# Kernel optimization log

Measured on AMD Instinct MI355X. Metric: run time of the kernel, lower is better.

Reference implementation:

```python
import jax, jax.numpy as jnp
import numpy as np

# Sizes derived from init_kwargs via calc_mlp_features:
# total_param=2117777, router_ratio=0.002 -> router_param=4235.554, expert_param=264192
# expert_hidden = 256, router_hidden = 352
N = 131072      # number of coordinate points
CIN = 3         # expert_insize == router_insize (xyz coords)
E = 8           # num_experts
K = 2           # top_k
H = 256         # expert_hidden (also SIREN data_channel)
RH = 352        # router_hidden
NHID = 3        # expert_layers - 2 hidden SIREN layers
W0C = 30.0      # sine frequency w0


def setup_inputs() -> dict:
    key = jax.random.key(0)
    ks = jax.random.split(key, 16)
    u = lambda k, shape, a: jax.random.uniform(k, shape, jnp.float32, -a, a)
    x = jax.random.uniform(ks[0], (N, CIN), jnp.float32, -1.0, 1.0)
    context = jax.random.uniform(ks[1], (N, CIN), jnp.float32, -1.0, 1.0)
    # Router: kaiming-normal weights, torch-default uniform biases
    Wr1 = jax.random.normal(ks[2], (CIN, RH), jnp.float32) * np.float32(np.sqrt(2.0 / CIN))
    br1 = u(ks[3], (RH,), 1.0 / np.sqrt(CIN))
    Wr2 = jax.random.normal(ks[4], (RH, E), jnp.float32) * np.float32(np.sqrt(2.0 / RH))
    br2 = u(ks[5], (E,), 1.0 / np.sqrt(RH))
    # SIREN experts (stacked over E): first layer U(-1/in, 1/in), rest U(+-sqrt(6/in)/30)
    sb = np.sqrt(6.0 / H) / 30.0
    W0 = u(ks[6], (E, CIN, H), 1.0 / CIN)
    b0 = u(ks[7], (E, H), 1.0 / np.sqrt(CIN))
    Wh = u(ks[8], (E, NHID, H, H), sb)
    bh = u(ks[9], (E, NHID, H), 1.0 / np.sqrt(H))
    Wo = u(ks[10], (E, H, H), sb)
    bo = u(ks[11], (E, H), 1.0 / np.sqrt(H))
    # Decoder: Linear(H,H)+ReLU+Linear(H,1)
    Wd1 = jax.random.normal(ks[12], (H, H), jnp.float32) * np.float32(np.sqrt(2.0 / H))
    bd1 = u(ks[13], (H,), 1.0 / np.sqrt(H))
    Wd2 = jax.random.normal(ks[14], (H, 1), jnp.float32) * np.float32(np.sqrt(2.0 / H))
    bd2 = u(ks[15], (1,), 1.0 / np.sqrt(H))
    return dict(x=x, context=context, Wr1=Wr1, br1=br1, Wr2=Wr2, br2=br2,
                W0=W0, b0=b0, Wh=Wh, bh=bh, Wo=Wo, bo=bo,
                Wd1=Wd1, bd1=bd1, Wd2=Wd2, bd2=bd2)


def reference(x, context, Wr1, br1, Wr2, br2, W0, b0, Wh, bh, Wo, bo, Wd1, bd1, Wd2, bd2):
    n = x.shape[0]
    # --- NoisyTopkRouter (eval path: no noise) ---
    logits = jnp.maximum(context @ Wr1 + br1, 0.0) @ Wr2 + br2          # [N, E]
    topv, topi = jax.lax.top_k(logits, K)                                # [N, K]
    # softmax over -inf-filled sparse logits == softmax over the top-k values
    w = jax.nn.softmax(topv, axis=-1)                                    # [N, K]
    gating = jnp.zeros_like(logits).at[jnp.arange(n)[:, None], topi].set(w)  # [N, E], zero off top-k
    # --- Per-expert SIREN, weighted combine ---
    # Masked dispatch + scatter-add in the original equals dense weighted sum
    # because gating is exactly zero for non-selected experts.
    def expert_step(acc, p):
        W0e, b0e, Whe, bhe, Woe, boe, ge = p
        h = jnp.sin(W0C * (x @ W0e + b0e))                # [N, H]
        for i in range(NHID):
            h = jnp.sin(W0C * (h @ Whe[i] + bhe[i]))
        out = h @ Woe + boe                               # [N, H], no output activation
        return acc + out * ge[:, None], None
    acc0 = jnp.zeros((n, H), dtype=x.dtype)
    final, _ = jax.lax.scan(expert_step, acc0, (W0, b0, Wh, bh, Wo, bo, gating.T))
    # --- Decoder ---
    return jnp.maximum(final @ Wd1 + bd1, 0.0) @ Wd2 + bd2               # [N, 1]
```

## Files before the change

kernel.cpp:

```cpp
#include <hip/hip_runtime.h>
#include <stdint.h>

#define N_PTS 131072
#define RH    352
#define BM    256
#define BME   64
#define TPB   512
#define SREV  4.774648292756860f

typedef short  bf16x8 __attribute__((ext_vector_type(8)));
typedef float  f32x16 __attribute__((ext_vector_type(16)));

__device__ __forceinline__ unsigned short f2bf(float f) {
  uint32_t u = __builtin_bit_cast(uint32_t, f);
  u = (u + 0x7FFFu + ((u >> 16) & 1u)) >> 16;
  return (unsigned short)u;
}
__device__ __forceinline__ float bf2f(unsigned short s) {
  return __builtin_bit_cast(float, ((uint32_t)s) << 16);
}
__device__ __forceinline__ float vsin1(float x) {
  float xf = x - floorf(x);
  float r;
  asm("v_sin_f32 %0, %1" : "=v"(r) : "v"(xf));
  return r;
}
__device__ __forceinline__ void ldsload16(const void* g, void* ldsWaveBase) {
  typedef __attribute__((address_space(3))) uint8_t lds_b;
  typedef __attribute__((address_space(1))) uint8_t glob_b;
  __builtin_amdgcn_global_load_lds((const glob_b*)g, (lds_b*)ldsWaveBase, 16, 0, 0);
}
__device__ __forceinline__ f32x16 mfma_bf16(bf16x8 a, bf16x8 b, f32x16 c) {
  return __builtin_amdgcn_mfma_f32_32x32x16_bf16(a, b, c, 0, 0, 0);
}

#define AWLOAD(d0, d1, addr64) \
  asm volatile("global_load_dwordx4 %0, %2, off\n\t" \
               "global_load_dwordx4 %1, %2, off offset:1024" \
               : "=&v"(d0), "=&v"(d1) : "v"(addr64))

#define VWAIT(N, r0, r1) \
  asm volatile("s_waitcnt vmcnt(" #N ")" : "+v"(r0), "+v"(r1))

__global__ __launch_bounds__(512) void pack_kernel(
    const float* __restrict__ W0, const float* __restrict__ b0,
    const float* __restrict__ Wh, const float* __restrict__ bh,
    const float* __restrict__ Wo, const float* __restrict__ bo,
    const float* __restrict__ Wd1, const float* __restrict__ bd1,
    short* __restrict__ pW0, short* __restrict__ pWh,
    short* __restrict__ pWo, short* __restrict__ pWd1)
{
  int b = blockIdx.x, tid = threadIdx.x;
  int jb = tid >> 6, l = tid & 63;
  int j  = jb*32 + (l & 31);
  int s0 = (l >> 5) * 8;
  unsigned short o[8];
  short* dp;

  if (b < 544) {
    int m = b / 17, slice = b % 17;
    int e = m >> 2, t = m & 3;
    const float* src; const float* bias; float scale; short* dst;
    if (t < 3) { src = Wh + (size_t)(e*3+t)*65536; bias = bh + (size_t)(e*3+t)*256; scale = SREV; dst = pWh + (size_t)(e*3+t)*69632; }
    else       { src = Wo + (size_t)e*65536;       bias = bo + (size_t)e*256;       scale = 1.0f; dst = pWo + (size_t)e*69632; }
    if (slice < 16) {
      #pragma unroll
      for (int i = 0; i < 8; ++i) {
        int k = slice*16 + s0 + i;
        o[i] = f2bf(scale * src[(size_t)k*256 + j]);
      }
    } else {
      #pragma unroll
      for (int i = 0; i < 8; ++i) o[i] = 0;
      if (s0 == 0) {
        float a = scale * bias[j];
        unsigned short h = f2bf(a);
        o[0] = h; o[1] = f2bf(a - bf2f(h));
      }
    }
    dp = dst + (size_t)slice*4096 + jb*512 + l*8;
  } else if (b < 552) {
    int e = b - 544;
    const float* w0 = W0 + (size_t)e*768;
    const float* bb = b0 + (size_t)e*256;
    #pragma unroll
    for (int i = 0; i < 8; ++i) {
      int s = s0 + i;
      unsigned short v = 0;
      if (s < 3) v = f2bf(SREV * w0[(size_t)s*256 + j]);
      else if (s < 6) { float a = SREV * w0[(size_t)(s-3)*256 + j]; unsigned short h = f2bf(a); v = f2bf(a - bf2f(h)); }
      else if (s < 9) v = f2bf(SREV * w0[(size_t)(s-6)*256 + j]);
      else if (s == 9)  v = f2bf(SREV * bb[j]);
      else if (s == 10) { float a = SREV * bb[j]; unsigned short h = f2bf(a); v = f2bf(a - bf2f(h)); }
      o[i] = v;
    }
    dp = pW0 + (size_t)e*4096 + jb*512 + l*8;
  } else {
    int slice = b - 552;
    if (slice < 16) {
      #pragma unroll
      for (int i = 0; i < 8; ++i) {
        int k = slice*16 + s0 + i;
        o[i] = f2bf(Wd1[(size_t)k*256 + j]);
      }
    } else {
      #pragma unroll
      for (int i = 0; i < 8; ++i) o[i] = 0;
      if (s0 == 0) {
        float a = bd1[j];
        unsigned short h = f2bf(a);
        o[0] = h; o[1] = f2bf(a - bf2f(h));
      }
    }
    dp = pWd1 + (size_t)slice*4096 + jb*512 + l*8;
  }
  uint4 v;
  v.x = (uint32_t)o[0] | ((uint32_t)o[1] << 16);
  v.y = (uint32_t)o[2] | ((uint32_t)o[3] << 16);
  v.z = (uint32_t)o[4] | ((uint32_t)o[5] << 16);
  v.w = (uint32_t)o[6] | ((uint32_t)o[7] << 16);
  *(uint4*)dp = v;
}

__global__ __launch_bounds__(256) void router_kernel(
    const float* __restrict__ ctx, const float* __restrict__ Wr1,
    const float* __restrict__ br1, const float* __restrict__ Wr2,
    const float* __restrict__ br2, uint4* __restrict__ topk,
    uint32_t* __restrict__ counts)
{
  __shared__ double w1d[RH*4];
  __shared__ double w2d[RH*8];
  __shared__ uint32_t lcnt[8];
  int tid = threadIdx.x;
  for (int i = tid; i < RH; i += 256) {
    w1d[i*4+0] = (double)Wr1[i];
    w1d[i*4+1] = (double)Wr1[352 + i];
    w1d[i*4+2] = (double)Wr1[704 + i];
    w1d[i*4+3] = (double)br1[i];
  }
  for (int i = tid; i < RH*8; i += 256) w2d[i] = (double)Wr2[i];
  if (tid < 8) lcnt[tid] = 0;
  __syncthreads();

  int n = blockIdx.x*256 + tid;
  double c0 = (double)ctx[(size_t)n*3+0];
  double c1 = (double)ctx[(size_t)n*3+1];
  double c2 = (double)ctx[(size_t)n*3+2];
  double lg[8];
  #pragma unroll
  for (int e = 0; e < 8; ++e) lg[e] = (double)br2[e];
  for (int j = 0; j < RH; ++j) {
    const double* a = &w1d[j*4];
    double h = c0*a[0] + c1*a[1] + c2*a[2] + a[3];
    h = h > 0.0 ? h : 0.0;
    const double* bq = &w2d[j*8];
    lg[0] += h*bq[0]; lg[1] += h*bq[1]; lg[2] += h*bq[2]; lg[3] += h*bq[3];
    lg[4] += h*bq[4]; lg[5] += h*bq[5]; lg[6] += h*bq[6]; lg[7] += h*bq[7];
  }
  double v0 = -1e300, v1 = -1e300; int i0 = 0, i1 = 0;
  #pragma unroll
  for (int e = 0; e < 8; ++e) {
    double lv = lg[e];
    if (lv > v0)      { v1 = v0; i1 = i0; v0 = lv; i0 = e; }
    else if (lv > v1) { v1 = lv; i1 = e; }
  }
  float ex = __expf((float)(v1 - v0));
  float s = 1.0f / (1.0f + ex);
  uint4 t;
  t.x = (uint32_t)i0 | ((uint32_t)i1 << 8);
  t.y = __builtin_bit_cast(uint32_t, s);
  t.z = __builtin_bit_cast(uint32_t, ex * s);
  t.w = 0;
  topk[n] = t;
  atomicAdd(&lcnt[i0], 1u); atomicAdd(&lcnt[i1], 1u);
  __syncthreads();
  if (tid < 8) atomicAdd(&counts[tid], lcnt[tid]);
}

__global__ void scan_kernel(const uint32_t* __restrict__ counts,
                            uint32_t* __restrict__ offsets,
                            uint32_t* __restrict__ cursors)
{
  if (threadIdx.x == 0) {
    uint32_t o = 0;
    for (int e = 0; e < 8; ++e) { offsets[e] = o; cursors[e] = o; o += counts[e]; }
    offsets[8] = o;
  }
}

__global__ __launch_bounds__(256) void scatter_kernel(
    const uint4* __restrict__ topk, uint32_t* __restrict__ cursors,
    uint32_t* __restrict__ plist, float* __restrict__ pw)
{
  __shared__ uint32_t lc[8], lb[8];
  int tid = threadIdx.x;
  if (tid < 8) lc[tid] = 0;
  __syncthreads();
  int n = blockIdx.x*256 + tid;
  uint4 t = topk[n];
  uint32_t e0 = t.x & 255u, e1 = (t.x >> 8) & 255u;
  uint32_t p0 = atomicAdd(&lc[e0], 1u);
  uint32_t p1 = atomicAdd(&lc[e1], 1u);
  __syncthreads();
  if (tid < 8) lb[tid] = atomicAdd(&cursors[tid], lc[tid]);
  __syncthreads();
  uint32_t d0 = lb[e0] + p0, d1 = lb[e1] + p1;
  plist[d0] = ((uint32_t)n << 1);      pw[d0] = __builtin_bit_cast(float, t.y);
  plist[d1] = ((uint32_t)n << 1) | 1u; pw[d1] = __builtin_bit_cast(float, t.z);
}

#define LDS_EXPERT 67584

__global__ __launch_bounds__(256, 2) void expert_kernel(
    const float* __restrict__ x, const uint32_t* __restrict__ counts,
    const uint32_t* __restrict__ offsets, const uint32_t* __restrict__ plist,
    const float* __restrict__ pw, const short* __restrict__ pW0,
    const short* __restrict__ pWh, const short* __restrict__ pWo,
    short* __restrict__ outbuf)
{
  extern __shared__ __align__(16) uint8_t smem[];
  uint8_t* hB0 = smem;
  uint8_t* hB1 = smem + 32768;
  uint8_t* xB  = smem + 65536;

  int tid = threadIdx.x;
  int lane = tid & 63;
  int jq = tid >> 6;
  int aoff = jq*2048 + lane*16;

  bf16x8 bbias;
  #pragma unroll
  for (int i = 0; i < 8; ++i) bbias[i] = 0;
  if (lane < 32) { bbias[0] = (short)0x3F80; bbias[1] = (short)0x3F80; }

  bf16x8 aw[5][2];
  f32x16 acc[2][2];

  int rr = tid >> 2;
  int rq = tid & 3;

  uint32_t tt = blockIdx.x;
  int e = -1; uint32_t cnt = 0;
  #pragma unroll 1
  for (int ee = 0; ee < 8; ++ee) {
    uint32_t c = counts[ee];
    uint32_t nt = (c + (BME-1)) >> 6;
    if (tt < nt) { e = ee; cnt = c; break; }
    tt -= nt;
  }
  if (e < 0) return;
  uint32_t base = offsets[e] + (tt << 6);
  int nvalid = (int)cnt - (int)(tt << 6); if (nvalid > BME) nvalid = BME;

  uint64_t matp[4];
  matp[0] = (uint64_t)(uintptr_t)(pWh + (size_t)(e*3+0)*69632);
  matp[1] = (uint64_t)(uintptr_t)(pWh + (size_t)(e*3+1)*69632);
  matp[2] = (uint64_t)(uintptr_t)(pWh + (size_t)(e*3+2)*69632);
  matp[3] = (uint64_t)(uintptr_t)(pWo + (size_t)e*69632);

  {
    uint64_t pb = matp[0] + (uint64_t)aoff;
    AWLOAD(aw[0][0], aw[0][1], pb);
    AWLOAD(aw[1][0], aw[1][1], pb + 8192);
    AWLOAD(aw[2][0], aw[2][1], pb + 16384);
    AWLOAD(aw[3][0], aw[3][1], pb + 24576);
  }

  float wgt[2];
  #pragma unroll
  for (int c = 0; c < 2; ++c) {
    int n = c*32 + (lane & 31);
    wgt[c] = (n < nvalid) ? pw[base + n] : 0.0f;
  }
  uint32_t psv = (rr < nvalid) ? plist[base + rr] : 0u;

  if (tid < BME) {
    float x0 = 0.0f, x1 = 0.0f, x2 = 0.0f;
    if (tid < nvalid) {
      uint32_t v = plist[base + tid];
      const float* xp = x + (size_t)(v >> 1)*3;
      x0 = xp[0]; x1 = xp[1]; x2 = xp[2];
    }
    unsigned short h0 = f2bf(x0), h1 = f2bf(x1), h2 = f2bf(x2);
    unsigned short l0 = f2bf(x0 - bf2f(h0)), l1 = f2bf(x1 - bf2f(h1)), l2 = f2bf(x2 - bf2f(h2));
    uint4 r0, r1;
    r0.x = (uint32_t)h0 | ((uint32_t)h1 << 16);
    r0.y = (uint32_t)h2 | ((uint32_t)h0 << 16);
    r0.z = (uint32_t)h1 | ((uint32_t)h2 << 16);
    r0.w = (uint32_t)l0 | ((uint32_t)l1 << 16);
    r1.x = (uint32_t)l2 | (0x3F80u << 16);
    r1.y = 0x3F80u;
    r1.z = 0u; r1.w = 0u;
    uint4* dst = (uint4*)(xB + tid*32);
    dst[0] = r0; dst[1] = r1;
  }

  const uint8_t* pw0e = (const uint8_t*)(pW0 + (size_t)e*4096);
  bf16x8 a0[2];
  a0[0] = *(const bf16x8*)(pw0e + aoff);
  a0[1] = *(const bf16x8*)(pw0e + aoff + 1024);

  __syncthreads();

  #pragma unroll
  for (int a2 = 0; a2 < 2; ++a2)
    #pragma unroll
    for (int c = 0; c < 2; ++c)
      #pragma unroll
      for (int r = 0; r < 16; ++r) acc[a2][c][r] = 0.0f;

  {
    bf16x8 bv[2];
    #pragma unroll
    for (int c = 0; c < 2; ++c) {
      int n = c*32 + (lane & 31);
      bv[c] = *(const bf16x8*)(xB + n*32 + ((lane >> 5)*16));
    }
    #pragma unroll
    for (int a2 = 0; a2 < 2; ++a2)
      #pragma unroll
      for (int c = 0; c < 2; ++c)
        acc[a2][c] = mfma_bf16(a0[a2], bv[c], acc[a2][c]);
  }

#define WRITE_SIN(HB) { _Pragma("unroll") \
    for (int a2 = 0; a2 < 2; ++a2) { \
      int jb = jq*2 + a2; \
      _Pragma("unroll") \
      for (int c = 0; c < 2; ++c) { \
        int n = c*32 + (lane & 31); \
        uint32_t rowb = (uint32_t)n * 512u; \
        uint32_t sw = (uint32_t)((n & 7) << 4); \
        _Pragma("unroll") \
        for (int g = 0; g < 4; ++g) { \
          float s0f = vsin1(acc[a2][c][g*4+0]); \
          float s1f = vsin1(acc[a2][c][g*4+1]); \
          float s2f = vsin1(acc[a2][c][g*4+2]); \
          float s3f = vsin1(acc[a2][c][g*4+3]); \
          uint2 pv; \
          pv.x = (uint32_t)f2bf(s0f) | ((uint32_t)f2bf(s1f) << 16); \
          pv.y = (uint32_t)f2bf(s2f) | ((uint32_t)f2bf(s3f) << 16); \
          int j0 = jb*32 + g*8 + ((lane >> 5) << 2); \
          uint32_t off = (rowb + (uint32_t)(j0*2)) ^ sw; \
          *(uint2*)((HB) + off) = pv; \
        } \
      } \
    } }

  WRITE_SIN(hB0);
  __syncthreads();

#define STEP(L, kb, HB) { \
    enum { u_ = (L)*17 + (kb), ps_ = u_ + 4, us_ = u_ % 5, pss_ = ps_ % 5 }; \
    if (ps_ <= 67) { \
      uint64_t pa_ = matp[ps_/17] + (uint64_t)((ps_%17)*8192) + (uint64_t)aoff; \
      AWLOAD(aw[pss_][0], aw[pss_][1], pa_); \
    } \
    if (u_ <= 63)      { VWAIT(8, aw[us_][0], aw[us_][1]); } \
    else if (u_ == 64) { VWAIT(6, aw[us_][0], aw[us_][1]); } \
    else if (u_ == 65) { VWAIT(4, aw[us_][0], aw[us_][1]); } \
    else if (u_ == 66) { VWAIT(2, aw[us_][0], aw[us_][1]); } \
    else               { VWAIT(0, aw[us_][0], aw[us_][1]); } \
    bf16x8 bv0_, bv1_; \
    if ((kb) < 16) { \
      { int n_ = (lane & 31); \
        uint32_t off_ = ((uint32_t)n_*512u + (uint32_t)((kb)*32) + (uint32_t)((lane >> 5)*16)) \
                        ^ (uint32_t)((n_ & 7) << 4); \
        bv0_ = *(const bf16x8*)((HB) + off_); } \
      { int n_ = 32 + (lane & 31); \
        uint32_t off_ = ((uint32_t)n_*512u + (uint32_t)((kb)*32) + (uint32_t)((lane >> 5)*16)) \
                        ^ (uint32_t)((n_ & 7) << 4); \
        bv1_ = *(const bf16x8*)((HB) + off_); } \
    } else { bv0_ = bbias; bv1_ = bbias; } \
    acc[0][0] = mfma_bf16(aw[us_][0], bv0_, acc[0][0]); \
    acc[1][0] = mfma_bf16(aw[us_][1], bv0_, acc[1][0]); \
    acc[0][1] = mfma_bf16(aw[us_][0], bv1_, acc[0][1]); \
    acc[1][1] = mfma_bf16(aw[us_][1], bv1_, acc[1][1]); \
}
#define LAYER17(L, HB) STEP(L,0,HB) STEP(L,1,HB) STEP(L,2,HB) STEP(L,3,HB) \
    STEP(L,4,HB) STEP(L,5,HB) STEP(L,6,HB) STEP(L,7,HB) STEP(L,8,HB) \
    STEP(L,9,HB) STEP(L,10,HB) STEP(L,11,HB) STEP(L,12,HB) STEP(L,13,HB) \
    STEP(L,14,HB) STEP(L,15,HB) STEP(L,16,HB)

#define ZACC() { _Pragma("unroll") for (int a2 = 0; a2 < 2; ++a2) \
    _Pragma("unroll") for (int c = 0; c < 2; ++c) \
    _Pragma("unroll") for (int r = 0; r < 16; ++r) acc[a2][c][r] = 0.0f; }

  ZACC(); LAYER17(0, hB0) WRITE_SIN(hB1); __syncthreads();
  ZACC(); LAYER17(1, hB1) WRITE_SIN(hB0); __syncthreads();
  ZACC(); LAYER17(2, hB0) WRITE_SIN(hB1); __syncthreads();
  ZACC(); LAYER17(3, hB1)
  #pragma unroll
  for (int a2 = 0; a2 < 2; ++a2) {
    int jb = jq*2 + a2;
    #pragma unroll
    for (int c = 0; c < 2; ++c) {
      int n = c*32 + (lane & 31);
      float w = wgt[c];
      uint32_t rowb = (uint32_t)n * 512u;
      uint32_t sw = (uint32_t)((n & 7) << 4);
      #pragma unroll
      for (int g = 0; g < 4; ++g) {
        float s0f = acc[a2][c][g*4+0] * w;
        float s1f = acc[a2][c][g*4+1] * w;
        float s2f = acc[a2][c][g*4+2] * w;
        float s3f = acc[a2][c][g*4+3] * w;
        uint2 pv;
        pv.x = (uint32_t)f2bf(s0f) | ((uint32_t)f2bf(s1f) << 16);
        pv.y = (uint32_t)f2bf(s2f) | ((uint32_t)f2bf(s3f) << 16);
        int j0 = jb*32 + g*8 + ((lane >> 5) << 2);
        uint32_t off = (rowb + (uint32_t)(j0*2)) ^ sw;
        *(uint2*)(hB0 + off) = pv;
      }
    }
  }
  __syncthreads();
  if (rr < nvalid) {
    uint4* dst = (uint4*)(outbuf + ((size_t)(psv & 1)*N_PTS + (size_t)(psv >> 1))*256
                          + rq*64);
    uint32_t rowb = (uint32_t)rr*512u + (uint32_t)rq*128u;
    uint32_t sw = (uint32_t)((rr & 7) << 4);
    #pragma unroll
    for (int c = 0; c < 8; ++c)
      dst[c] = *(const uint4*)(hB0 + ((rowb + (uint32_t)(c*16)) ^ sw));
  }
}

#define LDS_DEC 150528

__global__ __launch_bounds__(TPB, 2) void decoder_kernel(
    const short* __restrict__ outbuf, const short* __restrict__ pWd1,
    const float* __restrict__ Wd2v, const float* __restrict__ bd2,
    float* __restrict__ outp)
{
  extern __shared__ __align__(16) uint8_t smem[];
  uint8_t* hB = smem;
  uint8_t* wB = smem + 131072;
  float* wd2 = (float*)(smem + 147456);
  float* part = (float*)(smem + 148480);

  int tid = threadIdx.x;
  int lane = tid & 63;
  int wv = tid >> 6;
  int nw = wv & 3;
  int jw = wv >> 2;
  int tbase = blockIdx.x * BM;

  ldsload16((const uint8_t*)pWd1 + (size_t)tid*16, wB + (tid >> 6)*1024);
  if (tid < 256) wd2[tid] = Wd2v[tid];

  const short* o0 = outbuf + (size_t)tbase*256;
  const short* o1 = outbuf + ((size_t)N_PTS + tbase)*256;
  #pragma unroll 1
  for (int it = 0; it < 16; ++it) {
    int c = it*512 + tid;
    uint4 a  = *(const uint4*)(o0 + (size_t)c*8);
    uint4 bq = *(const uint4*)(o1 + (size_t)c*8);
    uint4 ov;
    uint32_t* ap = (uint32_t*)&a;
    uint32_t* bp = (uint32_t*)&bq;
    uint32_t* op = (uint32_t*)&ov;
    #pragma unroll
    for (int w = 0; w < 4; ++w) {
      uint32_t ua = ap[w], ub = bp[w];
      float f0 = bf2f((unsigned short)(ua & 0xFFFFu)) + bf2f((unsigned short)(ub & 0xFFFFu));
      float f1 = bf2f((unsigned short)(ua >> 16))     + bf2f((unsigned short)(ub >> 16));
      op[w] = (uint32_t)f2bf(f0) | ((uint32_t)f2bf(f1) << 16);
    }
    int n = c >> 5;
    uint32_t off = ((uint32_t)n*512u + (uint32_t)(c & 31)*16u) ^ (uint32_t)((n & 7) << 4);
    *(uint4*)(hB + off) = ov;
  }
  __syncthreads();

  f32x16 acc[4][2];
  #pragma unroll
  for (int a2 = 0; a2 < 4; ++a2)
    #pragma unroll
    for (int c = 0; c < 2; ++c)
      #pragma unroll
      for (int r = 0; r < 16; ++r) acc[a2][c][r] = 0.0f;
  bf16x8 bbias;
  #pragma unroll
  for (int i = 0; i < 8; ++i) bbias[i] = 0;
  if (lane < 32) { bbias[0] = (short)0x3F80; bbias[1] = (short)0x3F80; }

  #pragma unroll 1
  for (int kb = 0; kb < 17; ++kb) {
    if (kb < 16)
      ldsload16((const uint8_t*)(pWd1 + (size_t)(kb+1)*4096) + (size_t)tid*16,
                wB + ((kb+1) & 1)*8192 + (tid >> 6)*1024);
    const uint8_t* wcur = wB + (kb & 1)*8192;
    bf16x8 av[4];
    #pragma unroll
    for (int a2 = 0; a2 < 4; ++a2)
      av[a2] = *(const bf16x8*)(wcur + (jw*4 + a2)*1024 + lane*16);
    bf16x8 bv[2];
    if (kb < 16) {
      #pragma unroll
      for (int c = 0; c < 2; ++c) {
        int n = (nw*2 + c)*32 + (lane & 31);
        uint32_t off = ((uint32_t)n*512u + (uint32_t)kb*32u + (uint32_t)((lane >> 5)*16))
                       ^ (uint32_t)((n & 7) << 4);
        bv[c] = *(const bf16x8*)(hB + off);
      }
    } else {
      bv[0] = bbias; bv[1] = bbias;
    }
    #pragma unroll
    for (int a2 = 0; a2 < 4; ++a2)
      #pragma unroll
      for (int c = 0; c < 2; ++c)
        acc[a2][c] = mfma_bf16(av[a2], bv[c], acc[a2][c]);
    __syncthreads();
  }

  float p0 = 0.0f, p1 = 0.0f;
  #pragma unroll
  for (int a2 = 0; a2 < 4; ++a2) {
    int jb = jw*4 + a2;
    #pragma unroll
    for (int c = 0; c < 2; ++c) {
      #pragma unroll
      for (int r = 0; r < 16; ++r) {
        int j = jb*32 + (r & 3) + ((r >> 2) << 3) + ((lane >> 5) << 2);
        float v = acc[a2][c][r];
        v = v > 0.0f ? v : 0.0f;
        float t = v * wd2[j];
        if (c == 0) p0 += t; else p1 += t;
      }
    }
  }
  p0 += __shfl_xor(p0, 32);
  p1 += __shfl_xor(p1, 32);
  if (lane < 32) {
    part[jw*256 + (nw*2+0)*32 + lane] = p0;
    part[jw*256 + (nw*2+1)*32 + lane] = p1;
  }
  __syncthreads();
  if (tid < 256)
    outp[tbase + tid] = part[tid] + part[256 + tid] + bd2[0];
}

extern "C" void kernel_launch(void* const* d_in, const int* in_sizes, int n_in,
                              void* d_out, int out_size, void* d_ws, size_t ws_size,
                              hipStream_t stream) {
  const float* x   = (const float*)d_in[0];
  const float* ctx = (const float*)d_in[1];
  const float* Wr1 = (const float*)d_in[2];
  const float* br1 = (const float*)d_in[3];
  const float* Wr2 = (const float*)d_in[4];
  const float* br2 = (const float*)d_in[5];
  const float* W0  = (const float*)d_in[6];
  const float* b0  = (const float*)d_in[7];
  const float* Wh  = (const float*)d_in[8];
  const float* bh  = (const float*)d_in[9];
  const float* Wo  = (const float*)d_in[10];
  const float* bo  = (const float*)d_in[11];
  const float* Wd1 = (const float*)d_in[12];
  const float* bd1 = (const float*)d_in[13];
  const float* Wd2 = (const float*)d_in[14];
  const float* bd2 = (const float*)d_in[15];
  float* out = (float*)d_out;

  const size_t WS_COUNTS  = 0;
  const size_t WS_CURSORS = 256;
  const size_t WS_OFFSETS = 512;
  const size_t WS_TOPK    = 1024;
  const size_t WS_PLIST   = WS_TOPK  + (size_t)N_PTS*16;
  const size_t WS_PW      = WS_PLIST + (size_t)N_PTS*8;
  const size_t WS_PW0     = WS_PW    + (size_t)N_PTS*8;
  const size_t WS_PWH     = WS_PW0   + (size_t)8*8192;
  const size_t WS_PWO     = WS_PWH   + (size_t)24*139264;
  const size_t WS_PWD1    = WS_PWO   + (size_t)8*139264;
  const size_t WS_OUT     = WS_PWD1  + (size_t)139264;
  const size_t WS_END     = WS_OUT   + (size_t)2*N_PTS*256*2;

  if (ws_size < WS_END) {
    hipMemsetAsync(d_out, 0xFF, (size_t)out_size*4, stream);
    return;
  }

  uint8_t* ws = (uint8_t*)d_ws;
  uint32_t* counts  = (uint32_t*)(ws + WS_COUNTS);
  uint32_t* cursors = (uint32_t*)(ws + WS_CURSORS);
  uint32_t* offsets = (uint32_t*)(ws + WS_OFFSETS);
  uint4*    topk    = (uint4*)   (ws + WS_TOPK);
  uint32_t* plist   = (uint32_t*)(ws + WS_PLIST);
  float*    pw      = (float*)   (ws + WS_PW);
  short*    pW0     = (short*)   (ws + WS_PW0);
  short*    pWh     = (short*)   (ws + WS_PWH);
  short*    pWo     = (short*)   (ws + WS_PWO);
  short*    pWd1    = (short*)   (ws + WS_PWD1);
  short*    outbuf  = (short*)   (ws + WS_OUT);

  hipMemsetAsync(counts, 0, 32, stream);
  hipFuncSetAttribute((const void*)expert_kernel,
                      hipFuncAttributeMaxDynamicSharedMemorySize, LDS_EXPERT);
  hipFuncSetAttribute((const void*)decoder_kernel,
                      hipFuncAttributeMaxDynamicSharedMemorySize, LDS_DEC);

  pack_kernel   <<<569,  512, 0, stream>>>(W0, b0, Wh, bh, Wo, bo, Wd1, bd1,
                                           pW0, pWh, pWo, pWd1);
  router_kernel <<<512,  256, 0, stream>>>(ctx, Wr1, br1, Wr2, br2, topk, counts);
  scan_kernel   <<<1,     64, 0, stream>>>(counts, offsets, cursors);
  scatter_kernel<<<512,  256, 0, stream>>>(topk, cursors, plist, pw);
  expert_kernel <<<4104, 256, LDS_EXPERT, stream>>>(x, counts, offsets, plist, pw,
                                                    pW0, pWh, pWo, outbuf);
  decoder_kernel<<<512,  TPB, LDS_DEC, stream>>>(outbuf, pWd1, Wd2, bd2, out);
}
```

Measured before the change: 277.7 us.

## Ping-pong two 64-point subtiles per expert block to overlap sine with MFMA

Each expert block now handles 128 points as two 64-point subtiles, A and B, each with its own accumulators and LDS activation buffer. The layer phases alternate between the subtiles. While one subtile runs its MFMA k-steps, the sine and bf16 packing of the other subtile's previous layer is interleaved step by step, so transcendental and LDS-store work can hide under matrix work. The grid is halved accordingly. The cost is twice the accumulator registers, which risks spills or lower occupancy. Each weight chunk is streamed once per subtile instead of once per block, and the single-expert tail tiles are less evenly filled.

```diff
diff --git a/kernel.cpp b/kernel.cpp
--- a/kernel.cpp
+++ b/kernel.cpp
@@ -4,7 +4,6 @@
 #define N_PTS 131072
 #define RH    352
 #define BM    256
-#define BME   64
 #define TPB   512
 #define SREV  4.774648292756860f
 
@@ -209,7 +208,7 @@
   plist[d1] = ((uint32_t)n << 1) | 1u; pw[d1] = __builtin_bit_cast(float, t.z);
 }
 
-#define LDS_EXPERT 67584
+#define LDS_EXPERT 69632
 
 __global__ __launch_bounds__(256, 2) void expert_kernel(
     const float* __restrict__ x, const uint32_t* __restrict__ counts,
@@ -219,9 +218,10 @@
     short* __restrict__ outbuf)
 {
   extern __shared__ __align__(16) uint8_t smem[];
-  uint8_t* hB0 = smem;
-  uint8_t* hB1 = smem + 32768;
-  uint8_t* xB  = smem + 65536;
+  uint8_t* hA  = smem;
+  uint8_t* hBt = smem + 32768;
+  uint8_t* xA  = smem + 65536;
+  uint8_t* xBt = smem + 67584;
 
   int tid = threadIdx.x;
   int lane = tid & 63;
@@ -234,7 +234,8 @@
   if (lane < 32) { bbias[0] = (short)0x3F80; bbias[1] = (short)0x3F80; }
 
   bf16x8 aw[5][2];
-  f32x16 acc[2][2];
+  f32x16 accA[2][2];
+  f32x16 accB[2][2];
 
   int rr = tid >> 2;
   int rq = tid & 3;
@@ -244,13 +245,16 @@
   #pragma unroll 1
   for (int ee = 0; ee < 8; ++ee) {
     uint32_t c = counts[ee];
-    uint32_t nt = (c + (BME-1)) >> 6;
+    uint32_t nt = (c + 127u) >> 7;
     if (tt < nt) { e = ee; cnt = c; break; }
     tt -= nt;
   }
   if (e < 0) return;
-  uint32_t base = offsets[e] + (tt << 6);
-  int nvalid = (int)cnt - (int)(tt << 6); if (nvalid > BME) nvalid = BME;
+  uint32_t baseA = offsets[e] + (tt << 7);
+  uint32_t baseB = baseA + 64;
+  int rem = (int)cnt - (int)(tt << 7);
+  int nvA = rem > 64 ? 64 : rem;
+  int nvB = rem - 64; if (nvB < 0) nvB = 0; if (nvB > 64) nvB = 64;
 
   uint64_t matp[4];
   matp[0] = (uint64_t)(uintptr_t)(pWh + (size_t)(e*3+0)*69632);
@@ -266,18 +270,25 @@
     AWLOAD(aw[3][0], aw[3][1], pb + 24576);
   }
 
-  float wgt[2];
+  float wgtA[2], wgtB[2];
   #pragma unroll
   for (int c = 0; c < 2; ++c) {
     int n = c*32 + (lane & 31);
-    wgt[c] = (n < nvalid) ? pw[base + n] : 0.0f;
-  }
-  uint32_t psv = (rr < nvalid) ? plist[base + rr] : 0u;
-
-  if (tid < BME) {
+    wgtA[c] = (n < nvA) ? pw[baseA + n] : 0.0f;
+    wgtB[c] = (n < nvB) ? pw[baseB + n] : 0.0f;
+  }
+  uint32_t psvA = (rr < nvA) ? plist[baseA + rr] : 0u;
+  uint32_t psvB = (rr < nvB) ? plist[baseB + rr] : 0u;
+
+  if (tid < 128) {
+    int tl = tid & 63;
+    int isB = tid >> 6;
+    int nv = isB ? nvB : nvA;
+    uint32_t bse = isB ? baseB : baseA;
+    uint8_t* xb = isB ? xBt : xA;
     float x0 = 0.0f, x1 = 0.0f, x2 = 0.0f;
-    if (tid < nvalid) {
-      uint32_t v = plist[base + tid];
+    if (tl < nv) {
+      uint32_t v = plist[bse + tl];
       const float* xp = x + (size_t)(v >> 1)*3;
       x0 = xp[0]; x1 = xp[1]; x2 = xp[2];
     }
@@ -291,7 +302,7 @@
     r1.x = (uint32_t)l2 | (0x3F80u << 16);
     r1.y = 0x3F80u;
     r1.z = 0u; r1.w = 0u;
-    uint4* dst = (uint4*)(xB + tid*32);
+    uint4* dst = (uint4*)(xb + tl*32);
     dst[0] = r0; dst[1] = r1;
   }
 
@@ -302,127 +313,150 @@
 
   __syncthreads();
 
-  #pragma unroll
-  for (int a2 = 0; a2 < 2; ++a2)
-    #pragma unroll
-    for (int c = 0; c < 2; ++c)
-      #pragma unroll
-      for (int r = 0; r < 16; ++r) acc[a2][c][r] = 0.0f;
+#define ZACCX(ACC) { _Pragma("unroll") for (int a2 = 0; a2 < 2; ++a2) \
+    _Pragma("unroll") for (int c = 0; c < 2; ++c) \
+    _Pragma("unroll") for (int r = 0; r < 16; ++r) ACC[a2][c][r] = 0.0f; }
+
+  ZACCX(accA); ZACCX(accB);
 
   {
     bf16x8 bv[2];
     #pragma unroll
     for (int c = 0; c < 2; ++c) {
       int n = c*32 + (lane & 31);
-      bv[c] = *(const bf16x8*)(xB + n*32 + ((lane >> 5)*16));
+      bv[c] = *(const bf16x8*)(xA + n*32 + ((lane >> 5)*16));
     }
     #pragma unroll
     for (int a2 = 0; a2 < 2; ++a2)
       #pragma unroll
       for (int c = 0; c < 2; ++c)
-        acc[a2][c] = mfma_bf16(a0[a2], bv[c], acc[a2][c]);
-  }
-
-#define WRITE_SIN(HB) { _Pragma("unroll") \
-    for (int a2 = 0; a2 < 2; ++a2) { \
-      int jb = jq*2 + a2; \
-      _Pragma("unroll") \
-      for (int c = 0; c < 2; ++c) { \
-        int n = c*32 + (lane & 31); \
-        uint32_t rowb = (uint32_t)n * 512u; \
-        uint32_t sw = (uint32_t)((n & 7) << 4); \
-        _Pragma("unroll") \
-        for (int g = 0; g < 4; ++g) { \
-          float s0f = vsin1(acc[a2][c][g*4+0]); \
-          float s1f = vsin1(acc[a2][c][g*4+1]); \
-          float s2f = vsin1(acc[a2][c][g*4+2]); \
-          float s3f = vsin1(acc[a2][c][g*4+3]); \
-          uint2 pv; \
-          pv.x = (uint32_t)f2bf(s0f) | ((uint32_t)f2bf(s1f) << 16); \
-          pv.y = (uint32_t)f2bf(s2f) | ((uint32_t)f2bf(s3f) << 16); \
-          int j0 = jb*32 + g*8 + ((lane >> 5) << 2); \
-          uint32_t off = (rowb + (uint32_t)(j0*2)) ^ sw; \
-          *(uint2*)((HB) + off) = pv; \
-        } \
-      } \
-    } }
-
-  WRITE_SIN(hB0);
-  __syncthreads();
-
-#define STEP(L, kb, HB) { \
-    enum { u_ = (L)*17 + (kb), ps_ = u_ + 4, us_ = u_ % 5, pss_ = ps_ % 5 }; \
-    if (ps_ <= 67) { \
-      uint64_t pa_ = matp[ps_/17] + (uint64_t)((ps_%17)*8192) + (uint64_t)aoff; \
+        accA[a2][c] = mfma_bf16(a0[a2], bv[c], accA[a2][c]);
+    #pragma unroll
+    for (int c = 0; c < 2; ++c) {
+      int n = c*32 + (lane & 31);
+      bv[c] = *(const bf16x8*)(xBt + n*32 + ((lane >> 5)*16));
+    }
+    #pragma unroll
+    for (int a2 = 0; a2 < 2; ++a2)
+      #pragma unroll
+      for (int c = 0; c < 2; ++c)
+        accB[a2][c] = mfma_bf16(a0[a2], bv[c], accB[a2][c]);
+  }
+
+#define SINGROUP(ACC, HB, g2) { \
+  enum { a2_ = (g2)>>3, c_ = ((g2)>>2)&1, g_ = (g2)&3 }; \
+  int n_ = c_*32 + (lane & 31); \
+  uint32_t rowb_ = (uint32_t)n_*512u; \
+  uint32_t sw_ = (uint32_t)((n_ & 7) << 4); \
+  float s0f_ = vsin1(ACC[a2_][c_][g_*4+0]); \
+  float s1f_ = vsin1(ACC[a2_][c_][g_*4+1]); \
+  float s2f_ = vsin1(ACC[a2_][c_][g_*4+2]); \
+  float s3f_ = vsin1(ACC[a2_][c_][g_*4+3]); \
+  uint2 pv_; \
+  pv_.x = (uint32_t)f2bf(s0f_) | ((uint32_t)f2bf(s1f_) << 16); \
+  pv_.y = (uint32_t)f2bf(s2f_) | ((uint32_t)f2bf(s3f_) << 16); \
+  int j0_ = (jq*2 + a2_)*32 + g_*8 + ((lane >> 5) << 2); \
+  *(uint2*)((HB) + ((rowb_ + (uint32_t)(j0_*2)) ^ sw_)) = pv_; \
+}
+#define GATEGROUP(ACC, HB, WGT, g2) { \
+  enum { a2_ = (g2)>>3, c_ = ((g2)>>2)&1, g_ = (g2)&3 }; \
+  int n_ = c_*32 + (lane & 31); \
+  uint32_t rowb_ = (uint32_t)n_*512u; \
+  uint32_t sw_ = (uint32_t)((n_ & 7) << 4); \
+  float w_ = WGT[c_]; \
+  float s0f_ = ACC[a2_][c_][g_*4+0] * w_; \
+  float s1f_ = ACC[a2_][c_][g_*4+1] * w_; \
+  float s2f_ = ACC[a2_][c_][g_*4+2] * w_; \
+  float s3f_ = ACC[a2_][c_][g_*4+3] * w_; \
+  uint2 pv_; \
+  pv_.x = (uint32_t)f2bf(s0f_) | ((uint32_t)f2bf(s1f_) << 16); \
+  pv_.y = (uint32_t)f2bf(s2f_) | ((uint32_t)f2bf(s3f_) << 16); \
+  int j0_ = (jq*2 + a2_)*32 + g_*8 + ((lane >> 5) << 2); \
+  *(uint2*)((HB) + ((rowb_ + (uint32_t)(j0_*2)) ^ sw_)) = pv_; \
+}
+
+#define DO16(M) M(0) M(1) M(2) M(3) M(4) M(5) M(6) M(7) \
+                M(8) M(9) M(10) M(11) M(12) M(13) M(14) M(15)
+
+#define SGA(g) SINGROUP(accA, hA, g)
+#define SGB(g) SINGROUP(accB, hBt, g)
+#define GGA(g) GATEGROUP(accA, hA, wgtA, g)
+#define GGB(g) GATEGROUP(accB, hBt, wgtB, g)
+#define NOG(g)
+
+  DO16(SGA);
+  __syncthreads();
+
+#define PSTEP(P, kb, ACC, HBASE) { \
+    enum { u_ = (P)*17 + (kb), ps_ = u_ + 4, us_ = u_ % 5, pss_ = ps_ % 5, \
+           pm_ = (ps_/17) >> 1, psl_ = ps_ % 17 }; \
+    if (ps_ <= 135) { \
+      uint64_t pa_ = matp[pm_] + (uint64_t)(psl_*8192) + (uint64_t)aoff; \
       AWLOAD(aw[pss_][0], aw[pss_][1], pa_); \
     } \
-    if (u_ <= 63)      { VWAIT(8, aw[us_][0], aw[us_][1]); } \
-    else if (u_ == 64) { VWAIT(6, aw[us_][0], aw[us_][1]); } \
-    else if (u_ == 65) { VWAIT(4, aw[us_][0], aw[us_][1]); } \
-    else if (u_ == 66) { VWAIT(2, aw[us_][0], aw[us_][1]); } \
-    else               { VWAIT(0, aw[us_][0], aw[us_][1]); } \
+    if (u_ <= 131)      { VWAIT(8, aw[us_][0], aw[us_][1]); } \
+    else if (u_ == 132) { VWAIT(6, aw[us_][0], aw[us_][1]); } \
+    else if (u_ == 133) { VWAIT(4, aw[us_][0], aw[us_][1]); } \
+    else if (u_ == 134) { VWAIT(2, aw[us_][0], aw[us_][1]); } \
+    else                { VWAIT(0, aw[us_][0], aw[us_][1]); } \
     bf16x8 bv0_, bv1_; \
     if ((kb) < 16) { \
       { int n_ = (lane & 31); \
         uint32_t off_ = ((uint32_t)n_*512u + (uint32_t)((kb)*32) + (uint32_t)((lane >> 5)*16)) \
                         ^ (uint32_t)((n_ & 7) << 4); \
-        bv0_ = *(const bf16x8*)((HB) + off_); } \
+        bv0_ = *(const bf16x8*)((HBASE) + off_); } \
       { int n_ = 32 + (lane & 31); \
         uint32_t off_ = ((uint32_t)n_*512u + (uint32_t)((kb)*32) + (uint32_t)((lane >> 5)*16)) \
                         ^ (uint32_t)((n_ & 7) << 4); \
-        bv1_ = *(const bf16x8*)((HB) + off_); } \
+        bv1_ = *(const bf16x8*)((HBASE) + off_); } \
     } else { bv0_ = bbias; bv1_ = bbias; } \
-    acc[0][0] = mfma_bf16(aw[us_][0], bv0_, acc[0][0]); \
-    acc[1][0] = mfma_bf16(aw[us_][1], bv0_, acc[1][0]); \
-    acc[0][1] = mfma_bf16(aw[us_][0], bv1_, acc[0][1]); \
-    acc[1][1] = mfma_bf16(aw[us_][1], bv1_, acc[1][1]); \
-}
-#define LAYER17(L, HB) STEP(L,0,HB) STEP(L,1,HB) STEP(L,2,HB) STEP(L,3,HB) \
-    STEP(L,4,HB) STEP(L,5,HB) STEP(L,6,HB) STEP(L,7,HB) STEP(L,8,HB) \
-    STEP(L,9,HB) STEP(L,10,HB) STEP(L,11,HB) STEP(L,12,HB) STEP(L,13,HB) \
-    STEP(L,14,HB) STEP(L,15,HB) STEP(L,16,HB)
-
-#define ZACC() { _Pragma("unroll") for (int a2 = 0; a2 < 2; ++a2) \
-    _Pragma("unroll") for (int c = 0; c < 2; ++c) \
-    _Pragma("unroll") for (int r = 0; r < 16; ++r) acc[a2][c][r] = 0.0f; }
-
-  ZACC(); LAYER17(0, hB0) WRITE_SIN(hB1); __syncthreads();
-  ZACC(); LAYER17(1, hB1) WRITE_SIN(hB0); __syncthreads();
-  ZACC(); LAYER17(2, hB0) WRITE_SIN(hB1); __syncthreads();
-  ZACC(); LAYER17(3, hB1)
-  #pragma unroll
-  for (int a2 = 0; a2 < 2; ++a2) {
-    int jb = jq*2 + a2;
-    #pragma unroll
-    for (int c = 0; c < 2; ++c) {
-      int n = c*32 + (lane & 31);
-      float w = wgt[c];
-      uint32_t rowb = (uint32_t)n * 512u;
-      uint32_t sw = (uint32_t)((n & 7) << 4);
-      #pragma unroll
-      for (int g = 0; g < 4; ++g) {
-        float s0f = acc[a2][c][g*4+0] * w;
-        float s1f = acc[a2][c][g*4+1] * w;
-        float s2f = acc[a2][c][g*4+2] * w;
-        float s3f = acc[a2][c][g*4+3] * w;
-        uint2 pv;
-        pv.x = (uint32_t)f2bf(s0f) | ((uint32_t)f2bf(s1f) << 16);
-        pv.y = (uint32_t)f2bf(s2f) | ((uint32_t)f2bf(s3f) << 16);
-        int j0 = jb*32 + g*8 + ((lane >> 5) << 2);
-        uint32_t off = (rowb + (uint32_t)(j0*2)) ^ sw;
-        *(uint2*)(hB0 + off) = pv;
-      }
-    }
-  }
-  __syncthreads();
-  if (rr < nvalid) {
-    uint4* dst = (uint4*)(outbuf + ((size_t)(psv & 1)*N_PTS + (size_t)(psv >> 1))*256
+    ACC[0][0] = mfma_bf16(aw[us_][0], bv0_, ACC[0][0]); \
+    ACC[1][0] = mfma_bf16(aw[us_][1], bv0_, ACC[1][0]); \
+    ACC[0][1] = mfma_bf16(aw[us_][0], bv1_, ACC[0][1]); \
+    ACC[1][1] = mfma_bf16(aw[us_][1], bv1_, ACC[1][1]); \
+}
+
+#define PHASE(P, ACC, HBASE, GRP) \
+  ZACCX(ACC) \
+  PSTEP(P,0,ACC,HBASE)  GRP(0)  PSTEP(P,1,ACC,HBASE)  GRP(1)  \
+  PSTEP(P,2,ACC,HBASE)  GRP(2)  PSTEP(P,3,ACC,HBASE)  GRP(3)  \
+  PSTEP(P,4,ACC,HBASE)  GRP(4)  PSTEP(P,5,ACC,HBASE)  GRP(5)  \
+  PSTEP(P,6,ACC,HBASE)  GRP(6)  PSTEP(P,7,ACC,HBASE)  GRP(7)  \
+  PSTEP(P,8,ACC,HBASE)  GRP(8)  PSTEP(P,9,ACC,HBASE)  GRP(9)  \
+  PSTEP(P,10,ACC,HBASE) GRP(10) PSTEP(P,11,ACC,HBASE) GRP(11) \
+  PSTEP(P,12,ACC,HBASE) GRP(12) PSTEP(P,13,ACC,HBASE) GRP(13) \
+  PSTEP(P,14,ACC,HBASE) GRP(14) PSTEP(P,15,ACC,HBASE) GRP(15) \
+  PSTEP(P,16,ACC,HBASE) \
+  __syncthreads();
+
+  PHASE(0, accA, hA,  SGB)
+  PHASE(1, accB, hBt, SGA)
+  PHASE(2, accA, hA,  SGB)
+  PHASE(3, accB, hBt, SGA)
+  PHASE(4, accA, hA,  SGB)
+  PHASE(5, accB, hBt, SGA)
+  PHASE(6, accA, hA,  SGB)
+  PHASE(7, accB, hBt, GGA)
+
+  if (rr < nvA) {
+    uint4* dst = (uint4*)(outbuf + ((size_t)(psvA & 1)*N_PTS + (size_t)(psvA >> 1))*256
                           + rq*64);
     uint32_t rowb = (uint32_t)rr*512u + (uint32_t)rq*128u;
     uint32_t sw = (uint32_t)((rr & 7) << 4);
     #pragma unroll
     for (int c = 0; c < 8; ++c)
-      dst[c] = *(const uint4*)(hB0 + ((rowb + (uint32_t)(c*16)) ^ sw));
+      dst[c] = *(const uint4*)(hA + ((rowb + (uint32_t)(c*16)) ^ sw));
+  }
+  DO16(GGB);
+  __syncthreads();
+  if (rr < nvB) {
+    uint4* dst = (uint4*)(outbuf + ((size_t)(psvB & 1)*N_PTS + (size_t)(psvB >> 1))*256
+                          + rq*64);
+    uint32_t rowb = (uint32_t)rr*512u + (uint32_t)rq*128u;
+    uint32_t sw = (uint32_t)((rr & 7) << 4);
+    #pragma unroll
+    for (int c = 0; c < 8; ++c)
+      dst[c] = *(const uint4*)(hBt + ((rowb + (uint32_t)(c*16)) ^ sw));
   }
 }
 
@@ -605,7 +639,7 @@
   router_kernel <<<512,  256, 0, stream>>>(ctx, Wr1, br1, Wr2, br2, topk, counts);
   scan_kernel   <<<1,     64, 0, stream>>>(counts, offsets, cursors);
   scatter_kernel<<<512,  256, 0, stream>>>(topk, cursors, plist, pw);
-  expert_kernel <<<4104, 256, LDS_EXPERT, stream>>>(x, counts, offsets, plist, pw,
+  expert_kernel <<<2056, 256, LDS_EXPERT, stream>>>(x, counts, offsets, plist, pw,
                                                     pW0, pWh, pWo, outbuf);
   decoder_kernel<<<512,  TPB, LDS_DEC, stream>>>(outbuf, pWd1, Wd2, bd2, out);
 }
```

New measurement: 280.4 us. No clear change (+1.0%).
